# Performance work log

Hardware: AMD Instinct MI355X
Metric: run time of the kernel (lower is better)

The kernel has to match this reference:

```python
import jax, jax.numpy as jnp
import numpy as np

B, N, N_MELS = 8, 4096, 64
DIM, LAYERS, HEADS = 256, 4, 4
DIM_HEAD = DIM // HEADS      # 64
INNER = HEADS * DIM_HEAD     # 256
NB_FEAT = 256                # random features
FF_MULT = 4                  # performer_pytorch FeedForward default


def _ortho_projection(rows, cols, rng):
    # gaussian_orthogonal_random_matrix, scaling=0 (performer_pytorch default)
    blocks = []
    for _ in range((rows + cols - 1) // cols):
        q, _ = np.linalg.qr(rng.standard_normal((cols, cols)))
        blocks.append(q.T)
    mat = np.concatenate(blocks)[:rows]
    multiplier = np.linalg.norm(rng.standard_normal((rows, cols)), axis=1)
    return (mat * multiplier[:, None]).astype(np.float32)


def setup_inputs() -> dict:
    rng = np.random.default_rng(0)
    def w(*s, scale=0.02):
        return jnp.asarray(rng.standard_normal(s).astype(np.float32) * scale)
    G2 = 2 * DIM * FF_MULT  # GLU projection width = 2048
    return {
        "x": jnp.asarray(rng.standard_normal((B, N, N_MELS)).astype(np.float32)),
        "proj_w": w(N_MELS, DIM), "proj_b": jnp.zeros((DIM,), jnp.float32),
        "ln1_g": jnp.ones((LAYERS, DIM), jnp.float32), "ln1_b": jnp.zeros((LAYERS, DIM), jnp.float32),
        "wq": w(LAYERS, DIM, INNER), "bq": jnp.zeros((LAYERS, INNER), jnp.float32),
        "wk": w(LAYERS, DIM, INNER), "bk": jnp.zeros((LAYERS, INNER), jnp.float32),
        "wv": w(LAYERS, DIM, INNER), "bv": jnp.zeros((LAYERS, INNER), jnp.float32),
        "wo": w(LAYERS, INNER, DIM), "bo": jnp.zeros((LAYERS, DIM), jnp.float32),
        "ln2_g": jnp.ones((LAYERS, DIM), jnp.float32), "ln2_b": jnp.zeros((LAYERS, DIM), jnp.float32),
        "w1": w(LAYERS, DIM, G2), "b1": jnp.zeros((LAYERS, G2), jnp.float32),
        "w2": w(LAYERS, DIM * FF_MULT, DIM), "b2": jnp.zeros((LAYERS, DIM), jnp.float32),
        "clf_w": w(DIM, 1), "clf_b": jnp.zeros((1,), jnp.float32),
        "proj_mat": jnp.asarray(_ortho_projection(NB_FEAT, DIM_HEAD, rng)),
    }


def _layer_norm(x, g, b, eps=1e-5):
    mu = jnp.mean(x, -1, keepdims=True)
    var = jnp.mean((x - mu) ** 2, -1, keepdims=True)
    return (x - mu) * jax.lax.rsqrt(var + eps) * g + b


def _softmax_kernel(data, proj, is_query, eps=1e-4):
    # FAVOR+ positive random features for softmax (performer_pytorch.softmax_kernel)
    dn = data.shape[-1] ** -0.25          # data_normalizer
    ratio = proj.shape[0] ** -0.5
    dd = jnp.einsum('bhnd,md->bhnm', data * dn, proj)
    diag = jnp.sum(data ** 2, -1, keepdims=True) * 0.5 * (dn ** 2)
    if is_query:
        m = jax.lax.stop_gradient(jnp.max(dd, axis=-1, keepdims=True))
    else:
        m = jax.lax.stop_gradient(jnp.max(dd))
    return ratio * (jnp.exp(dd - diag - m) + eps)


def _split_heads(t):
    b, n, _ = t.shape
    return t.reshape(b, n, HEADS, DIM_HEAD).transpose(0, 2, 1, 3)  # b h n d


def _forward(x, proj_w, proj_b, ln1_g, ln1_b, wq, bq, wk, bk, wv, bv, wo, bo,
             ln2_g, ln2_b, w1, b1, w2, b2, clf_w, clf_b, proj_mat):
    h = x @ proj_w + proj_b                       # [B, N, DIM]
    b, n = h.shape[0], h.shape[1]
    for l in range(LAYERS):
        # --- pre-LN self-attention (FAVOR+, non-causal) ---
        y = _layer_norm(h, ln1_g[l], ln1_b[l])
        q = _split_heads(y @ wq[l] + bq[l])
        k = _split_heads(y @ wk[l] + bk[l])
        v = _split_heads(y @ wv[l] + bv[l])
        qp = _softmax_kernel(q, proj_mat, is_query=True)    # [b,h,n,m]
        kp = _softmax_kernel(k, proj_mat, is_query=False)   # [b,h,n,m]
        d_inv = 1.0 / jnp.einsum('bhnm,bhm->bhn', qp, kp.sum(axis=2))
        ctx = jnp.einsum('bhnm,bhnd->bhmd', kp, v)          # [b,h,m,d]
        o = jnp.einsum('bhmd,bhnm,bhn->bhnd', ctx, qp, d_inv)
        o = o.transpose(0, 2, 1, 3).reshape(b, n, INNER)
        h = h + (o @ wo[l] + bo[l])
        # --- pre-LN GLU feed-forward ---
        y = _layer_norm(h, ln2_g[l], ln2_b[l])
        u = y @ w1[l] + b1[l]
        a, g = jnp.split(u, 2, axis=-1)
        h = h + (jax.nn.gelu(a, approximate=False) * g) @ w2[l] + b2[l]
    # clf: transpose + AdaptiveAvgPool1d(1) == mean over time, then Linear(dim,1)
    pooled = h.mean(axis=1)                       # [B, DIM]
    return (pooled @ clf_w + clf_b)[:, 0]         # [B]


def reference(x, proj_w, proj_b, ln1_g, ln1_b, wq, bq, wk, bk, wv, bv, wo, bo,
              ln2_g, ln2_b, w1, b1, w2, b2, clf_w, clf_b, proj_mat):
    return _forward(x, proj_w, proj_b, ln1_g, ln1_b, wq, bq, wk, bk, wv, bv,
                    wo, bo, ln2_g, ln2_b, w1, b1, w2, b2, clf_w, clf_b, proj_mat)
```

## Files before the change

### kernel.cpp

```cpp
#include <hip/hip_runtime.h>
#include <cstdint>
#include <cstddef>

constexpr float DN = 0.35355339059327373f;
constexpr float RATIO = 0.0625f;
constexpr float EPSF = 1e-4f;

typedef __attribute__((ext_vector_type(8))) short short8;
typedef __attribute__((ext_vector_type(8))) _Float16 half8;
typedef __attribute__((ext_vector_type(4))) float f32x4;

constexpr size_t OFF_H     = 0;
constexpr size_t OFF_YS    = 33554432;
constexpr size_t OFF_WTS   = 50331648;
constexpr size_t OFF_QK    = 67108864;
constexpr size_t OFF_BIG   = 100663296;
constexpr size_t OFF_VT    = 167772160;
constexpr size_t OFF_CTXP  = 188743680;
constexpr size_t OFF_CTXTH = 199229440;
constexpr size_t OFF_DIAGQ = 201850880;
constexpr size_t OFF_DIAGK = 202375168;
constexpr size_t OFF_GMAX  = 203423744;
constexpr size_t OFF_POOL  = 203424000;
constexpr size_t OFF_PMTH  = 207749376;
constexpr size_t OFF_PWTH  = 207814912;
constexpr size_t OFF_PWTL  = 207847680;
constexpr size_t WS_BYTES  = 207880448;

constexpr size_t WQF = 0;
constexpr size_t WKF = 65536;
constexpr size_t WVF = 131072;
constexpr size_t WOF = 196608;
constexpr size_t W1F = 262144;
constexpr size_t W2F = 786432;

__device__ __forceinline__ unsigned fkey(float f) {
    unsigned u = __float_as_uint(f);
    return (u & 0x80000000u) ? ~u : (u | 0x80000000u);
}
__device__ __forceinline__ float funkey(unsigned k) {
    unsigned u = (k & 0x80000000u) ? (k ^ 0x80000000u) : ~k;
    return __uint_as_float(u);
}
__device__ __forceinline__ float gelu_exact(float x) {
    return 0.5f * x * (1.0f + erff(x * 0.70710678118654752f));
}
__device__ __forceinline__ void splitf(float x, unsigned short& h, unsigned short& l) {
    unsigned u = __float_as_uint(x);
    unsigned hv = (u + 0x7FFFu + ((u >> 16) & 1)) >> 16;
    h = (unsigned short)hv;
    float lo = x - __uint_as_float(hv << 16);
    unsigned u2 = __float_as_uint(lo);
    l = (unsigned short)((u2 + 0x7FFFu + ((u2 >> 16) & 1)) >> 16);
}
__device__ __forceinline__ unsigned short bf16rne(float x) {
    unsigned u = __float_as_uint(x);
    return (unsigned short)((u + 0x7FFFu + ((u >> 16) & 1)) >> 16);
}
__device__ __forceinline__ unsigned short fp16rne(float x) {
    return __builtin_bit_cast(unsigned short, (_Float16)x);
}
template<bool F16>
__device__ __forceinline__ f32x4 mfma16(short8 a, short8 b, f32x4 c) {
    if constexpr (F16)
        return __builtin_amdgcn_mfma_f32_16x16x32_f16(
            __builtin_bit_cast(half8, a), __builtin_bit_cast(half8, b), c, 0, 0, 0);
    else
        return __builtin_amdgcn_mfma_f32_16x16x32_bf16(a, b, c, 0, 0, 0);
}
__device__ __forceinline__ void xcd_swz(int& bx, int& by) {
    const int gx = gridDim.x;
    const int total = gx * gridDim.y;
    int flat = blockIdx.y * gx + blockIdx.x;
    flat = (flat & 7) * (total >> 3) + (flat >> 3);
    bx = flat % gx; by = flat / gx;
}

#if defined(__has_builtin)
#if __has_builtin(__builtin_amdgcn_global_load_lds)
#define HAVE_GLDS 1
#endif
#endif
__device__ __forceinline__ void glds16(const unsigned short* g, unsigned short* l) {
#ifdef HAVE_GLDS
    __builtin_amdgcn_global_load_lds(
        (const __attribute__((address_space(1))) unsigned int*)g,
        (__attribute__((address_space(3))) unsigned int*)l, 16, 0, 0);
#else
    *(uint4*)l = *(const uint4*)g;
#endif
}

__global__ void fill_sentinel(float* out, int n) {
    int i = threadIdx.x;
    if (i < n) out[i] = 12345.0f;
}
__global__ __launch_bounds__(256) void vt_init(unsigned short* __restrict__ vT, unsigned* __restrict__ gm) {
    int i = blockIdx.x * 256 + threadIdx.x;
    if (i < 4) gm[i] = 0u;
    const int bh = i >> 13;
    const int r = (i >> 9) & 15;
    const unsigned val = (r == 0) ? 0x3C003C00u : 0u;
    uint4 q; q.x = val; q.y = val; q.z = val; q.w = val;
    *(uint4*)(vT + ((size_t)bh * 80 + 64 + r) * 4096 + ((size_t)(i & 511) << 3)) = q;
}

__global__ __launch_bounds__(256) void split_scale(
    const float* __restrict__ src, unsigned short* __restrict__ hi,
    unsigned short* __restrict__ lo, int n, float scale)
{
    int i = blockIdx.x * 256 + threadIdx.x;
    if (i < n) {
        unsigned short h, l;
        splitf(src[i] * scale, h, l);
        hi[i] = h; lo[i] = l;
    }
}

__global__ __launch_bounds__(256) void tofp16_scale(
    const float* __restrict__ src, unsigned short* __restrict__ dst, int n, float scale)
{
    int i = blockIdx.x * 256 + threadIdx.x;
    if (i < n) dst[i] = fp16rne(src[i] * scale);
}

__global__ __launch_bounds__(256) void splitT(
    const float* __restrict__ W, unsigned short* __restrict__ hi,
    unsigned short* __restrict__ lo, int kshift, int N)
{
    int i = blockIdx.x * 256 + threadIdx.x;
    int K = 1 << kshift;
    int n = i >> kshift, k = i & (K - 1);
    unsigned short h, l;
    splitf(W[(size_t)k * N + n], h, l);
    hi[i] = h; lo[i] = l;
}

__global__ __launch_bounds__(256) void split_weights(
    const float* __restrict__ wq, const float* __restrict__ wk,
    const float* __restrict__ wv, const float* __restrict__ wo,
    const float* __restrict__ w1, const float* __restrict__ w2,
    unsigned short* __restrict__ dst)
{
    const int i = blockIdx.x * 256 + threadIdx.x;
    const int lay = i >> 20;
    const int r = i & 1048575;
    float val; size_t oh;
    if (r < 262144) {
        const int m = r >> 16, e = r & 65535;
        const int n = e >> 8, k = e & 255;
        const float* W = (m == 0 ? wq : m == 1 ? wk : m == 2 ? wv : wo);
        val = W[(size_t)lay * 65536 + k * 256 + n];
        oh = (size_t)lay * 1048576 + (size_t)m * 65536 + e;
    } else if (r < 786432) {
        const int e = r - 262144;
        const int n = e >> 8, k = e & 255;
        val = w1[(size_t)lay * 524288 + (size_t)k * 2048 + n];
        oh = (size_t)lay * 1048576 + W1F + e;
    } else {
        const int e = r - 786432;
        const int n = e >> 10, k = e & 1023;
        val = w2[(size_t)lay * 262144 + (size_t)k * 256 + n];
        oh = (size_t)lay * 1048576 + W2F + e;
    }
    dst[oh] = fp16rne(val);
}

__global__ __launch_bounds__(256) void ln_f16(
    const float* __restrict__ x, const float* __restrict__ g,
    const float* __restrict__ b, unsigned short* __restrict__ yhi)
{
    const int row = blockIdx.x * 4 + (threadIdx.x >> 6);
    const int lane = threadIdx.x & 63;
    float4 t = *(const float4*)&x[(size_t)row * 256 + lane * 4];
    float s = t.x + t.y + t.z + t.w;
#pragma unroll
    for (int sh = 1; sh < 64; sh <<= 1) s += __shfl_xor(s, sh);
    const float mu = s * (1.0f / 256.0f);
    const float dx = t.x - mu, dy = t.y - mu, dz = t.z - mu, dw = t.w - mu;
    float vv = dx * dx + dy * dy + dz * dz + dw * dw;
#pragma unroll
    for (int sh = 1; sh < 64; sh <<= 1) vv += __shfl_xor(vv, sh);
    const float rstd = rsqrtf(vv * (1.0f / 256.0f) + 1e-5f);
    float4 gv = *(const float4*)&g[lane * 4];
    float4 bv = *(const float4*)&b[lane * 4];
    unsigned short h0 = fp16rne(dx * rstd * gv.x + bv.x);
    unsigned short h1 = fp16rne(dy * rstd * gv.y + bv.y);
    unsigned short h2 = fp16rne(dz * rstd * gv.z + bv.z);
    unsigned short h3 = fp16rne(dw * rstd * gv.w + bv.w);
    uint2 ph;
    ph.x = (unsigned)h0 | ((unsigned)h1 << 16); ph.y = (unsigned)h2 | ((unsigned)h3 << 16);
    *(uint2*)&yhi[(size_t)row * 256 + lane * 4] = ph;
}

template<int EPI, bool ASPLIT, bool BSPLIT, bool F16>
__global__ __launch_bounds__(256) void gemm_mf(
    const unsigned short* __restrict__ Ahi, const unsigned short* __restrict__ Alo, int lda,
    const unsigned short* __restrict__ Bhi, const unsigned short* __restrict__ Blo, int ldb,
    int K,
    const float* __restrict__ bias, const float* __restrict__ res,
    float* __restrict__ C, int ldc,
    unsigned short* __restrict__ Obf,
    const float* __restrict__ diag, unsigned* __restrict__ keys)
{
    constexpr int NP = (ASPLIT ? 2 : 1) + (BSPLIT ? 2 : 1);
    constexpr int PB = ASPLIT ? 2 : 1;
    constexpr int NEED = (EPI == 6) ? 16384 : 0;
    constexpr int LDSN = (NP * 8192 > NEED) ? NP * 8192 : NEED;
    __shared__ unsigned short lds[LDSN];
    __shared__ float red[4];
#define LX(p, h, r, c) lds[(p) * 8192 + (h) * 4096 + (r) * 32 + (c)]
    int bx, by; xcd_swz(bx, by);
    const int tid = threadIdx.x;
    const int m0 = by * 128, n0 = bx * 128;
    const int sr = tid >> 2, sc = (tid & 3) * 8;
    const unsigned short* ga_h = Ahi + (size_t)(m0 + sr) * lda + sc;
    const unsigned short* ga_l = ASPLIT ? (Alo + (size_t)(m0 + sr) * lda + sc) : nullptr;
    const unsigned short* gb_h = Bhi + (size_t)(n0 + sr) * ldb + sc;
    const unsigned short* gb_l = BSPLIT ? (Blo + (size_t)(n0 + sr) * ldb + sc) : nullptr;
    unsigned short* lp = lds + tid * 8;
    const int l = tid & 63, w = tid >> 6;
    const int wr = (w >> 1) * 64, wc = (w & 1) * 64;
    const int fr = l & 15, fq = l >> 4;

    f32x4 acc[4][4];
#pragma unroll
    for (int i = 0; i < 4; ++i)
#pragma unroll
        for (int j = 0; j < 4; ++j) acc[i][j] = (f32x4){0.f, 0.f, 0.f, 0.f};

    for (int k0 = 0; k0 < K; k0 += 64) {
        glds16(ga_h + k0, lp);
        glds16(ga_h + (size_t)64 * lda + k0, lp + 2048);
        glds16(ga_h + k0 + 32, lp + 4096);
        glds16(ga_h + (size_t)64 * lda + k0 + 32, lp + 6144);
        if (ASPLIT) {
            glds16(ga_l + k0, lp + 8192);
            glds16(ga_l + (size_t)64 * lda + k0, lp + 10240);
            glds16(ga_l + k0 + 32, lp + 12288);
            glds16(ga_l + (size_t)64 * lda + k0 + 32, lp + 14336);
        }
        glds16(gb_h + k0, lp + PB * 8192);
        glds16(gb_h + (size_t)64 * ldb + k0, lp + PB * 8192 + 2048);
        glds16(gb_h + k0 + 32, lp + PB * 8192 + 4096);
        glds16(gb_h + (size_t)64 * ldb + k0 + 32, lp + PB * 8192 + 6144);
        if (BSPLIT) {
            glds16(gb_l + k0, lp + (PB + 1) * 8192);
            glds16(gb_l + (size_t)64 * ldb + k0, lp + (PB + 1) * 8192 + 2048);
            glds16(gb_l + k0 + 32, lp + (PB + 1) * 8192 + 4096);
            glds16(gb_l + (size_t)64 * ldb + k0 + 32, lp + (PB + 1) * 8192 + 6144);
        }
        __syncthreads();
#pragma unroll
        for (int h2 = 0; h2 < 2; ++h2) {
            short8 ah[4], al[4];
#pragma unroll
            for (int mf = 0; mf < 4; ++mf) {
                ah[mf] = *(const short8*)&LX(0, h2, wr + mf * 16 + fr, fq * 8);
                if (ASPLIT) al[mf] = *(const short8*)&LX(1, h2, wr + mf * 16 + fr, fq * 8);
            }
#pragma unroll
            for (int nf = 0; nf < 4; ++nf) {
                short8 bh = *(const short8*)&LX(PB, h2, wc + nf * 16 + fr, fq * 8);
#pragma unroll
                for (int mf = 0; mf < 4; ++mf) {
                    acc[mf][nf] = mfma16<F16>(ah[mf], bh, acc[mf][nf]);
                    if (ASPLIT) acc[mf][nf] = mfma16<F16>(al[mf], bh, acc[mf][nf]);
                }
                if (BSPLIT) {
                    short8 bl = *(const short8*)&LX(PB + 1, h2, wc + nf * 16 + fr, fq * 8);
#pragma unroll
                    for (int mf = 0; mf < 4; ++mf)
                        acc[mf][nf] = mfma16<F16>(ah[mf], bl, acc[mf][nf]);
                }
            }
        }
        __syncthreads();
    }

    if constexpr (EPI == 4) {
        float m = -3.4e38f;
#pragma unroll
        for (int mf = 0; mf < 4; ++mf)
#pragma unroll
            for (int nf = 0; nf < 4; ++nf)
#pragma unroll
                for (int v = 0; v < 4; ++v) m = fmaxf(m, acc[mf][nf][v]);
#pragma unroll
        for (int s = 1; s < 64; s <<= 1) m = fmaxf(m, __shfl_xor(m, s));
        if (l == 0) red[w] = m;
        __syncthreads();
        if (tid == 0)
            atomicMax(keys, fkey(fmaxf(fmaxf(red[0], red[1]), fmaxf(red[2], red[3]))));
    } else if constexpr (EPI == 6) {
        const float Mg = funkey(*keys);
        unsigned short* tb = lds;
#pragma unroll
        for (int mf = 0; mf < 4; ++mf)
#pragma unroll
            for (int v = 0; v < 4; ++v) {
                const int rl = wr + mf * 16 + fq * 4 + v;
                const float dg = diag[m0 + rl] + Mg;
#pragma unroll
                for (int nf = 0; nf < 4; ++nf) {
                    const int cl = wc + nf * 16 + fr;
                    tb[rl * 128 + cl] = fp16rne(RATIO * (__expf(acc[mf][nf][v] - dg) + EPSF));
                }
            }
        __syncthreads();
        const int tokbase = m0 >> 2;
        const int b = tokbase >> 12, nib = tokbase & 4095;
        const int ml = tid & 127, g2 = tid >> 7;
#pragma unroll
        for (int hh2 = 0; hh2 < 2; ++hh2) {
            const int hh = g2 * 2 + hh2;
            unsigned short* dst = Obf + ((size_t)((b * 4 + hh) * 256 + n0 + ml)) * 4096 + nib;
#pragma unroll
            for (int qq = 0; qq < 4; ++qq) {
                uint4 qv;
                unsigned wv[4];
#pragma unroll
                for (int j = 0; j < 4; ++j) {
                    unsigned s0 = tb[((qq * 8 + j * 2 + 0) * 4 + hh) * 128 + ml];
                    unsigned s1 = tb[((qq * 8 + j * 2 + 1) * 4 + hh) * 128 + ml];
                    wv[j] = s0 | (s1 << 16);
                }
                qv.x = wv[0]; qv.y = wv[1]; qv.z = wv[2]; qv.w = wv[3];
                *(uint4*)(dst + qq * 8) = qv;
            }
        }
    } else {
#pragma unroll
        for (int nf = 0; nf < 4; ++nf) {
            const int col = n0 + wc + nf * 16 + fr;
            float bb = 0.f;
            if (bias != nullptr) bb = bias[col];
#pragma unroll
            for (int mf = 0; mf < 4; ++mf) {
#pragma unroll
                for (int v = 0; v < 4; ++v) {
                    const int row = m0 + wr + mf * 16 + fq * 4 + v;
                    const size_t off = (size_t)row * ldc + col;
                    float val = acc[mf][nf][v] + bb;
                    if (EPI == 1) val += res[off];
                    C[off] = val;
                }
            }
        }
    }
#undef LX
}

__global__ __launch_bounds__(256) void gemm_qkv(
    const unsigned short* __restrict__ A, const unsigned short* __restrict__ wl,
    const float* __restrict__ bq, const float* __restrict__ bk, const float* __restrict__ bv,
    unsigned short* __restrict__ vT, unsigned short* __restrict__ khi,
    unsigned short* __restrict__ qhi, float* __restrict__ diagq, float* __restrict__ diagk)
{
    __shared__ unsigned short lds[16384];
    int bx, by; xcd_swz(bx, by);
    const int sel = by >> 8;
    const int m0 = (by & 255) * 128, n0 = bx * 128;
    const unsigned short* Bw = wl + (sel == 0 ? WVF : sel == 1 ? WKF : WQF);
    const float* bias = (sel == 0 ? bv : sel == 1 ? bk : bq);
    const int tid = threadIdx.x;
    const int sr = tid >> 2, sc = (tid & 3) * 8;
    const unsigned short* ga = A + (size_t)(m0 + sr) * 256 + sc;
    const unsigned short* gb = Bw + (size_t)(n0 + sr) * 256 + sc;
    unsigned short* lp = lds + tid * 8;
    const int l = tid & 63, w = tid >> 6;
    const int wr = (w >> 1) * 64, wc = (w & 1) * 64;
    const int fr = l & 15, fq = l >> 4;

    f32x4 acc[4][4];
#pragma unroll
    for (int i = 0; i < 4; ++i)
#pragma unroll
        for (int j = 0; j < 4; ++j) acc[i][j] = (f32x4){0.f, 0.f, 0.f, 0.f};

    for (int k0 = 0; k0 < 256; k0 += 64) {
        glds16(ga + k0, lp);
        glds16(ga + (size_t)64 * 256 + k0, lp + 2048);
        glds16(ga + k0 + 32, lp + 4096);
        glds16(ga + (size_t)64 * 256 + k0 + 32, lp + 6144);
        glds16(gb + k0, lp + 8192);
        glds16(gb + (size_t)64 * 256 + k0, lp + 10240);
        glds16(gb + k0 + 32, lp + 12288);
        glds16(gb + (size_t)64 * 256 + k0 + 32, lp + 14336);
        __syncthreads();
#pragma unroll
        for (int h2 = 0; h2 < 2; ++h2) {
            short8 ah[4];
#pragma unroll
            for (int mf = 0; mf < 4; ++mf)
                ah[mf] = *(const short8*)&lds[h2 * 4096 + (wr + mf * 16 + fr) * 32 + fq * 8];
#pragma unroll
            for (int nf = 0; nf < 4; ++nf) {
                short8 bh = *(const short8*)&lds[8192 + h2 * 4096 + (wc + nf * 16 + fr) * 32 + fq * 8];
#pragma unroll
                for (int mf = 0; mf < 4; ++mf)
                    acc[mf][nf] = mfma16<true>(ah[mf], bh, acc[mf][nf]);
            }
        }
        __syncthreads();
    }

    if (sel == 0) {
        unsigned short* tb = lds;
#pragma unroll
        for (int mf = 0; mf < 4; ++mf)
#pragma unroll
            for (int nf = 0; nf < 4; ++nf) {
                const int cl = wc + nf * 16 + fr;
                const float bb = bias[n0 + cl];
#pragma unroll
                for (int v = 0; v < 4; ++v) {
                    const int rl = wr + mf * 16 + fq * 4 + v;
                    tb[rl * 128 + cl] = fp16rne(acc[mf][nf][v] + bb);
                }
            }
        __syncthreads();
        const int b = m0 >> 12, nib = m0 & 4095;
        const int cl = tid & 127, half = tid >> 7;
        const int ch = n0 + cl, hh = ch >> 6, d = ch & 63;
        unsigned short* dst = vT + ((size_t)((b * 4 + hh) * 80 + d)) * 4096 + nib + half * 64;
#pragma unroll
        for (int qq = 0; qq < 8; ++qq) {
            uint4 qv;
            unsigned wv[4];
#pragma unroll
            for (int j = 0; j < 4; ++j) {
                unsigned s0 = tb[(half * 64 + qq * 8 + j * 2 + 0) * 128 + cl];
                unsigned s1 = tb[(half * 64 + qq * 8 + j * 2 + 1) * 128 + cl];
                wv[j] = s0 | (s1 << 16);
            }
            qv.x = wv[0]; qv.y = wv[1]; qv.z = wv[2]; qv.w = wv[3];
            *(uint4*)(dst + qq * 8) = qv;
        }
    } else {
        float* diag = (sel == 1 ? diagk : diagq);
        unsigned short* Obf = (sel == 1 ? khi : qhi);
        const int head = (n0 + wc) >> 6;
#pragma unroll
        for (int mf = 0; mf < 4; ++mf) {
            float sq[4] = {0.f, 0.f, 0.f, 0.f};
#pragma unroll
            for (int nf = 0; nf < 4; ++nf) {
                const int col = n0 + wc + nf * 16 + fr;
                const float bb = bias[col];
#pragma unroll
                for (int v = 0; v < 4; ++v) {
                    const int row = m0 + wr + mf * 16 + fq * 4 + v;
                    float val = acc[mf][nf][v] + bb;
                    Obf[(size_t)row * 256 + col] = fp16rne(val);
                    sq[v] += val * val;
                }
            }
#pragma unroll
            for (int v = 0; v < 4; ++v) {
                float s = sq[v];
                s += __shfl_xor(s, 1); s += __shfl_xor(s, 2);
                s += __shfl_xor(s, 4); s += __shfl_xor(s, 8);
                if (fr == 0)
                    diag[(size_t)(m0 + wr + mf * 16 + fq * 4 + v) * 4 + head] = s * 0.0625f;
            }
        }
    }
}

__global__ __launch_bounds__(256) void gemm_glu(
    const unsigned short* __restrict__ Ahi, const unsigned short* __restrict__ Wf,
    const float* __restrict__ b1, unsigned short* __restrict__ Obf)
{
    __shared__ unsigned short ldsA[8192];
    __shared__ unsigned short ldsB[8192];
    int bx, by; xcd_swz(bx, by);
    const int tid = threadIdx.x;
    const int m0 = by * 128, p0 = bx * 64;
    const int sr = tid >> 2, sc = (tid & 3) * 8;
    const unsigned short* ga  = Ahi + (size_t)(m0 + sr) * 256 + sc;
    const unsigned short* gba = Wf + (size_t)(p0 + sr) * 256 + sc;
    const unsigned short* gbg = Wf + (size_t)(1024 + p0 + sr) * 256 + sc;
    unsigned short* lpA = ldsA + tid * 8;
    unsigned short* lpB = ldsB + tid * 8;
    const int l = tid & 63, w = tid >> 6;
    const int wr = (w >> 1) * 64, wc = (w & 1) * 32;
    const int fr = l & 15, fq = l >> 4;

    f32x4 aa[4][2], ag[4][2];
#pragma unroll
    for (int i = 0; i < 4; ++i)
#pragma unroll
        for (int j = 0; j < 2; ++j) {
            aa[i][j] = (f32x4){0.f, 0.f, 0.f, 0.f};
            ag[i][j] = (f32x4){0.f, 0.f, 0.f, 0.f};
        }

    for (int k0 = 0; k0 < 256; k0 += 64) {
        glds16(ga + k0, lpA);
        glds16(ga + 64 * 256 + k0, lpA + 2048);
        glds16(ga + k0 + 32, lpA + 4096);
        glds16(ga + 64 * 256 + k0 + 32, lpA + 6144);
        glds16(gba + k0, lpB);
        glds16(gba + k0 + 32, lpB + 2048);
        glds16(gbg + k0, lpB + 4096);
        glds16(gbg + k0 + 32, lpB + 6144);
        __syncthreads();
#pragma unroll
        for (int h2 = 0; h2 < 2; ++h2) {
            short8 ah[4];
#pragma unroll
            for (int mf = 0; mf < 4; ++mf)
                ah[mf] = *(const short8*)&ldsA[h2 * 4096 + (wr + mf * 16 + fr) * 32 + fq * 8];
#pragma unroll
            for (int nf = 0; nf < 2; ++nf) {
                const int br_ = h2 * 2048 + (wc + nf * 16 + fr) * 32 + fq * 8;
                short8 bva = *(const short8*)&ldsB[br_];
                short8 bvg = *(const short8*)&ldsB[4096 + br_];
#pragma unroll
                for (int mf = 0; mf < 4; ++mf) {
                    aa[mf][nf] = mfma16<true>(ah[mf], bva, aa[mf][nf]);
                    ag[mf][nf] = mfma16<true>(ah[mf], bvg, ag[mf][nf]);
                }
            }
        }
        __syncthreads();
    }
#pragma unroll
    for (int nf = 0; nf < 2; ++nf) {
        const int ch = p0 + wc + nf * 16 + fr;
        const float ba = b1[ch], bg = b1[1024 + ch];
#pragma unroll
        for (int mf = 0; mf < 4; ++mf) {
#pragma unroll
            for (int v = 0; v < 4; ++v) {
                const int row = m0 + wr + mf * 16 + fq * 4 + v;
                float u = aa[mf][nf][v] + ba, g = ag[mf][nf][v] + bg;
                Obf[(size_t)row * 1024 + ch] = fp16rne(gelu_exact(u) * g);
            }
        }
    }
}

__global__ __launch_bounds__(256) void ctx_mfma(
    const unsigned short* __restrict__ kpT, const unsigned short* __restrict__ vT,
    float* __restrict__ ctxp)
{
    __shared__ unsigned short la[4096];
    __shared__ unsigned short lb[5120];
    int bx, by; xcd_swz(bx, by);
    const int bh = by, mt = bx & 3, kc = bx >> 2;
    const int tid = threadIdx.x;
    const int l = tid & 63, w = tid >> 6;
    const int wr = w * 16, fr = l & 15, fq = l >> 4;
    const int sr = tid >> 2, sc = (tid & 3) * 8;
    const unsigned short* ga  = kpT + ((size_t)bh * 256 + mt * 64 + sr) * 4096 + kc * 1024 + sc;
    const unsigned short* gb  = vT + ((size_t)bh * 80 + sr) * 4096 + kc * 1024 + sc;
    const unsigned short* gb2 = vT + ((size_t)bh * 80 + 64 + sr) * 4096 + kc * 1024 + sc;

    f32x4 acc[5];
#pragma unroll
    for (int j = 0; j < 5; ++j) acc[j] = (f32x4){0.f, 0.f, 0.f, 0.f};

    for (int k0 = 0; k0 < 1024; k0 += 64) {
        glds16(ga + k0, la + tid * 8);
        glds16(ga + k0 + 32, la + 2048 + tid * 8);
        glds16(gb + k0, lb + tid * 8);
        glds16(gb + k0 + 32, lb + 2560 + tid * 8);
        if (tid < 64) {
            glds16(gb2 + k0, lb + 2048 + tid * 8);
            glds16(gb2 + k0 + 32, lb + 2560 + 2048 + tid * 8);
        }
        __syncthreads();
#pragma unroll
        for (int h2 = 0; h2 < 2; ++h2) {
            short8 av = *(const short8*)&la[h2 * 2048 + (wr + fr) * 32 + fq * 8];
#pragma unroll
            for (int nf = 0; nf < 5; ++nf) {
                short8 bv = *(const short8*)&lb[h2 * 2560 + (nf * 16 + fr) * 32 + fq * 8];
                acc[nf] = mfma16<true>(av, bv, acc[nf]);
            }
        }
        __syncthreads();
    }
#pragma unroll
    for (int v = 0; v < 4; ++v) {
        const int row = mt * 64 + wr + fq * 4 + v;
#pragma unroll
        for (int nf = 0; nf < 5; ++nf)
            ctxp[((size_t)(kc * 32 + bh) * 256 + row) * 80 + nf * 16 + fr] = acc[nf][v];
    }
}

__global__ __launch_bounds__(256) void ctx_fix(
    const float* __restrict__ ctxp, unsigned short* __restrict__ cth)
{
    __shared__ float s[64][81];
    const int m0 = blockIdx.x * 64, bh = blockIdx.y;
    const int tid = threadIdx.x;
    for (int i = tid; i < 5120; i += 256) {
        const int ml = i / 80, dc = i % 80;
        float sum = 0.f;
#pragma unroll
        for (int kc = 0; kc < 4; ++kc)
            sum += ctxp[((size_t)(kc * 32 + bh) * 256 + m0 + ml) * 80 + dc];
        s[ml][dc] = sum;
    }
    __syncthreads();
    for (int i = tid; i < 5120; i += 256) {
        const int dc = i >> 6, ml = i & 63;
        cth[((size_t)bh * 80 + dc) * 256 + m0 + ml] = fp16rne(s[ml][dc]);
    }
}

__global__ __launch_bounds__(256) void qo_mfma(
    const unsigned short* __restrict__ qhi, const unsigned short* __restrict__ pmh,
    const unsigned short* __restrict__ cth, const float* __restrict__ diagq,
    unsigned short* __restrict__ osh)
{
    __shared__ unsigned short lds[16384 + 2560];
    __shared__ float rmax4[64][4];
    int bx, by; xcd_swz(bx, by);
    const int bh = by, b = bh >> 2, hh = bh & 3;
    const int t0 = bx * 64;
    const int tid = threadIdx.x;
    const int l = tid & 63, w = tid >> 6;
    const int fr = l & 15, fq = l >> 4;

    const int wc1 = w * 64;
    f32x4 a1[4][4];
#pragma unroll
    for (int i = 0; i < 4; ++i)
#pragma unroll
        for (int j = 0; j < 4; ++j) a1[i][j] = (f32x4){0.f, 0.f, 0.f, 0.f};

    const unsigned short* gq = qhi + (size_t)(b * 4096 + t0) * 256 + hh * 64;
#pragma unroll
    for (int ks = 0; ks < 2; ++ks) {
        const int k0 = ks * 32;
        glds16(gq + (size_t)(tid >> 2) * 256 + k0 + (tid & 3) * 8, lds + tid * 8);
#pragma unroll
        for (int i2 = 0; i2 < 4; ++i2) {
            const int c = tid + i2 * 256;
            glds16(pmh + (size_t)(c >> 2) * 64 + k0 + (c & 3) * 8, lds + 2048 + c * 8);
        }
        __syncthreads();
        short8 av[4];
#pragma unroll
        for (int mf = 0; mf < 4; ++mf)
            av[mf] = *(const short8*)&lds[(mf * 16 + fr) * 32 + fq * 8];
#pragma unroll
        for (int nf = 0; nf < 4; ++nf) {
            short8 bh_ = *(const short8*)&lds[2048 + (wc1 + nf * 16 + fr) * 32 + fq * 8];
#pragma unroll
            for (int mf = 0; mf < 4; ++mf)
                a1[mf][nf] = mfma16<true>(av[mf], bh_, a1[mf][nf]);
        }
        __syncthreads();
    }
#pragma unroll
    for (int mf = 0; mf < 4; ++mf)
#pragma unroll
        for (int v = 0; v < 4; ++v) {
            float rm = a1[mf][0][v];
#pragma unroll
            for (int nf = 1; nf < 4; ++nf) rm = fmaxf(rm, a1[mf][nf][v]);
            rm = fmaxf(rm, __shfl_xor(rm, 1));
            rm = fmaxf(rm, __shfl_xor(rm, 2));
            rm = fmaxf(rm, __shfl_xor(rm, 4));
            rm = fmaxf(rm, __shfl_xor(rm, 8));
            if (fr == 0) rmax4[mf * 16 + fq * 4 + v][w] = rm;
        }
    __syncthreads();
#pragma unroll
    for (int mf = 0; mf < 4; ++mf)
#pragma unroll
        for (int v = 0; v < 4; ++v) {
            const int tok = mf * 16 + fq * 4 + v;
            const float dg = diagq[(size_t)(b * 4096 + t0 + tok) * 4 + hh]
                           + fmaxf(fmaxf(rmax4[tok][0], rmax4[tok][1]),
                                   fmaxf(rmax4[tok][2], rmax4[tok][3]));
#pragma unroll
            for (int nf = 0; nf < 4; ++nf) {
                const int m = wc1 + nf * 16 + fr;
                lds[tok * 256 + (m ^ ((tok & 7) << 3))] =
                    fp16rne(RATIO * (__expf(a1[mf][nf][v] - dg) + EPSF));
            }
        }
    __syncthreads();

    unsigned short* lds2 = lds + 16384;
    f32x4 a2[5];
#pragma unroll
    for (int j = 0; j < 5; ++j) a2[j] = (f32x4){0.f, 0.f, 0.f, 0.f};
    const size_t bbase = (size_t)bh * 80 * 256;

    for (int k0 = 0; k0 < 256; k0 += 32) {
        glds16(cth + bbase + (size_t)(tid >> 2) * 256 + k0 + (tid & 3) * 8, lds2 + tid * 8);
        if (tid < 64) {
            const int c = 256 + tid;
            glds16(cth + bbase + (size_t)(c >> 2) * 256 + k0 + (c & 3) * 8, lds2 + c * 8);
        }
        __syncthreads();
        const int tok = w * 16 + fr;
        const int c = ((k0 >> 3) + fq) ^ (tok & 7);
        short8 av = *(const short8*)&lds[tok * 256 + c * 8];
#pragma unroll
        for (int nf = 0; nf < 5; ++nf) {
            short8 bvh = *(const short8*)&lds2[(nf * 16 + fr) * 32 + fq * 8];
            a2[nf] = mfma16<true>(av, bvh, a2[nf]);
        }
        __syncthreads();
    }
#pragma unroll
    for (int v = 0; v < 4; ++v) {
        const float den = __shfl(a2[4][v], (int)(l & 48));
        const float dinv = 1.0f / den;
        const int tok = w * 16 + fq * 4 + v;
        const size_t obase = (size_t)(b * 4096 + t0 + tok) * 256 + hh * 64;
#pragma unroll
        for (int nf = 0; nf < 4; ++nf)
            osh[obase + nf * 16 + fr] = fp16rne(a2[nf][v] * dinv);
    }
}

__global__ __launch_bounds__(256) void pool1_kernel(const float* __restrict__ h, float* __restrict__ part)
{
    const int b = blockIdx.x >> 4, ch = blockIdx.x & 15;
    const int tid = threadIdx.x;
    float acc = 0.f;
    for (int n = 0; n < 256; ++n)
        acc += h[((size_t)(b * 4096 + ch * 256 + n)) * 256 + tid];
    part[(size_t)blockIdx.x * 256 + tid] = acc;
}

__global__ __launch_bounds__(256) void pool2_kernel(
    const float* __restrict__ part, const float* __restrict__ cw,
    const float* __restrict__ cb, float* __restrict__ out)
{
    const int b = blockIdx.x, tid = threadIdx.x;
    float acc = 0.f;
#pragma unroll
    for (int c = 0; c < 16; ++c) acc += part[(size_t)(b * 16 + c) * 256 + tid];
    float val = acc * (1.0f / 4096.0f) * cw[tid];
#pragma unroll
    for (int s = 1; s < 64; s <<= 1) val += __shfl_xor(val, s);
    __shared__ float red[4];
    if ((tid & 63) == 0) red[tid >> 6] = val;
    __syncthreads();
    if (tid == 0) out[b] = red[0] + red[1] + red[2] + red[3] + cb[0];
}

extern "C" void kernel_launch(void* const* d_in, const int* in_sizes, int n_in,
                              void* d_out, int out_size, void* d_ws, size_t ws_size,
                              hipStream_t stream)
{
    (void)in_sizes; (void)n_in;
    if (ws_size < WS_BYTES) {
        fill_sentinel<<<1, 64, 0, stream>>>((float*)d_out, out_size);
        return;
    }

    const float* x     = (const float*)d_in[0];
    const float* projw = (const float*)d_in[1];
    const float* projb = (const float*)d_in[2];
    const float* ln1g  = (const float*)d_in[3];
    const float* ln1b  = (const float*)d_in[4];
    const float* wq    = (const float*)d_in[5];
    const float* bq    = (const float*)d_in[6];
    const float* wk    = (const float*)d_in[7];
    const float* bk    = (const float*)d_in[8];
    const float* wv    = (const float*)d_in[9];
    const float* bv    = (const float*)d_in[10];
    const float* wo    = (const float*)d_in[11];
    const float* bo    = (const float*)d_in[12];
    const float* ln2g  = (const float*)d_in[13];
    const float* ln2b  = (const float*)d_in[14];
    const float* w1    = (const float*)d_in[15];
    const float* b1    = (const float*)d_in[16];
    const float* w2    = (const float*)d_in[17];
    const float* b2    = (const float*)d_in[18];
    const float* clfw  = (const float*)d_in[19];
    const float* clfb  = (const float*)d_in[20];
    const float* projm = (const float*)d_in[21];

    char* WS = (char*)d_ws;
    float* h            = (float*)(WS + OFF_H);
    unsigned short* ysh = (unsigned short*)(WS + OFF_YS);
    unsigned short* wts = (unsigned short*)(WS + OFF_WTS);
    unsigned short* khi = (unsigned short*)(WS + OFF_QK);
    unsigned short* qhi = khi + 8388608;
    unsigned short* big = (unsigned short*)(WS + OFF_BIG);
    unsigned short* vT  = (unsigned short*)(WS + OFF_VT);
    float* ctxp         = (float*)(WS + OFF_CTXP);
    unsigned short* cth = (unsigned short*)(WS + OFF_CTXTH);
    float* diagq        = (float*)(WS + OFF_DIAGQ);
    float* diagk        = (float*)(WS + OFF_DIAGK);
    unsigned* gmax      = (unsigned*)(WS + OFF_GMAX);
    float* pool         = (float*)(WS + OFF_POOL);
    unsigned short* pmt_h = (unsigned short*)(WS + OFF_PMTH);
    unsigned short* pwt_h = (unsigned short*)(WS + OFF_PWTH);
    unsigned short* pwt_l = (unsigned short*)(WS + OFF_PWTL);
    unsigned short* xsh = big;
    unsigned short* xsl = big + 2097152;
    unsigned short* kpT = big;
    unsigned short* ffb = big;
    unsigned short* osh = ysh;

    split_scale<<<8192, 256, 0, stream>>>(x, xsh, xsl, 2097152, 1.0f);
    splitT<<<64, 256, 0, stream>>>(projw, pwt_h, pwt_l, 6, 256);
    tofp16_scale<<<64, 256, 0, stream>>>(projm, pmt_h, 16384, DN);
    vt_init<<<1024, 256, 0, stream>>>(vT, gmax);
    split_weights<<<16384, 256, 0, stream>>>(wq, wk, wv, wo, w1, w2, wts);
    gemm_mf<0, true, true, false><<<dim3(2, 256), 256, 0, stream>>>(xsh, xsl, 64,
        pwt_h, pwt_l, 64, 64, projb, nullptr, h, 256, nullptr, nullptr, nullptr);

    for (int l = 0; l < 4; ++l) {
        unsigned short* wl = wts + (size_t)l * 1048576;

        ln_f16<<<8192, 256, 0, stream>>>(h, ln1g + l * 256, ln1b + l * 256, ysh);
        gemm_qkv<<<dim3(2, 768), 256, 0, stream>>>(ysh, wl,
            bq + l * 256, bk + l * 256, bv + l * 256, vT, khi, qhi, diagq, diagk);
        gemm_mf<4, false, false, true><<<dim3(2, 1024), 256, 0, stream>>>(khi, nullptr, 64,
            pmt_h, nullptr, 64, 64, nullptr, nullptr, nullptr, 256, nullptr, nullptr, gmax + l);
        gemm_mf<6, false, false, true><<<dim3(2, 1024), 256, 0, stream>>>(khi, nullptr, 64,
            pmt_h, nullptr, 64, 64, nullptr, nullptr, nullptr, 256, kpT, diagk, gmax + l);
        ctx_mfma<<<dim3(16, 32), 256, 0, stream>>>(kpT, vT, ctxp);
        ctx_fix<<<dim3(4, 32), 256, 0, stream>>>(ctxp, cth);
        qo_mfma<<<dim3(64, 32), 256, 0, stream>>>(qhi, pmt_h, cth, diagq, osh);
        gemm_mf<1, false, false, true><<<dim3(2, 256), 256, 0, stream>>>(osh, nullptr, 256,
            wl + WOF, nullptr, 256, 256, bo + l * 256, h, h, 256, nullptr, nullptr, nullptr);

        ln_f16<<<8192, 256, 0, stream>>>(h, ln2g + l * 256, ln2b + l * 256, ysh);
        gemm_glu<<<dim3(16, 256), 256, 0, stream>>>(ysh, wl + W1F,
            b1 + (size_t)l * 2048, ffb);
        gemm_mf<1, false, false, true><<<dim3(2, 256), 256, 0, stream>>>(ffb, nullptr, 1024,
            wl + W2F, nullptr, 1024, 1024, b2 + l * 256, h, h, 256, nullptr, nullptr, nullptr);
    }

    pool1_kernel<<<128, 256, 0, stream>>>(h, pool);
    pool2_kernel<<<8, 256, 0, stream>>>(pool, clfw, clfb, (float*)d_out);
}
```

Before: 1.173 ms.

## Fuse residual GEMMs with following LayerNorm and use polynomial erf in GELU

Adds a 512-thread GEMM kernel that computes a full 128x256 row tile for the Wo and W2 projections, adds bias and residual, writes h, then reduces mean and variance across the tile in LDS and emits the next LayerNorm output as fp16. This removes the separate ln_f16 launches and their extra read of h inside the layer loop. GELU switches from erff to an Abramowitz-Stegun polynomial with __expf, which lowers the cost of the GLU epilogue but adds approximation error of roughly 1e-7. The residual path in the generic GEMM epilogue is dropped, and the last layer computes a LayerNorm that is never used.

```diff
diff --git a/kernel.cpp b/kernel.cpp
--- a/kernel.cpp
+++ b/kernel.cpp
@@ -42,8 +42,16 @@
     unsigned u = (k & 0x80000000u) ? (k ^ 0x80000000u) : ~k;
     return __uint_as_float(u);
 }
-__device__ __forceinline__ float gelu_exact(float x) {
-    return 0.5f * x * (1.0f + erff(x * 0.70710678118654752f));
+__device__ __forceinline__ float erf_fast(float x) {
+    float ax = fabsf(x);
+    float t = 1.0f / fmaf(0.3275911f, ax, 1.0f);
+    float p = t * fmaf(t, fmaf(t, fmaf(t, fmaf(t, 1.061405429f, -1.453152027f),
+                                      1.421413741f), -0.284496736f), 0.254829592f);
+    float r = 1.0f - p * __expf(-ax * ax);
+    return copysignf(r, x);
+}
+__device__ __forceinline__ float gelu_fast(float x) {
+    return 0.5f * x * (1.0f + erf_fast(x * 0.70710678118654752f));
 }
 __device__ __forceinline__ void splitf(float x, unsigned short& h, unsigned short& l) {
     unsigned u = __float_as_uint(x);
@@ -341,14 +349,127 @@
                 for (int v = 0; v < 4; ++v) {
                     const int row = m0 + wr + mf * 16 + fq * 4 + v;
                     const size_t off = (size_t)row * ldc + col;
-                    float val = acc[mf][nf][v] + bb;
-                    if (EPI == 1) val += res[off];
-                    C[off] = val;
+                    C[off] = acc[mf][nf][v] + bb;
                 }
             }
         }
     }
 #undef LX
+}
+
+__global__ __launch_bounds__(512) void gemm_w_ln(
+    const unsigned short* __restrict__ A, int lda, int K,
+    const unsigned short* __restrict__ W,
+    const float* __restrict__ bias, float* __restrict__ h,
+    const float* __restrict__ lng, const float* __restrict__ lnb,
+    unsigned short* __restrict__ ysh)
+{
+    __shared__ unsigned short ldsA[8192];
+    __shared__ unsigned short ldsB[16384];
+    int flat = blockIdx.x;
+    flat = (flat & 7) * ((int)gridDim.x >> 3) + (flat >> 3);
+    const int m0 = flat * 128;
+    const int tid = threadIdx.x;
+    const int sr = tid >> 2, sc = (tid & 3) * 8;
+    const unsigned short* ga = A + (size_t)(m0 + sr) * lda + sc;
+    const unsigned short* gb = W + (size_t)sr * K + sc;
+    unsigned short* lpA = ldsA + tid * 8;
+    const int l = tid & 63, w = tid >> 6;
+    const int wr = (w >> 2) * 64, wc = (w & 3) * 64;
+    const int fr = l & 15, fq = l >> 4;
+
+    f32x4 acc[4][4];
+#pragma unroll
+    for (int i = 0; i < 4; ++i)
+#pragma unroll
+        for (int j = 0; j < 4; ++j) acc[i][j] = (f32x4){0.f, 0.f, 0.f, 0.f};
+
+    for (int k0 = 0; k0 < K; k0 += 64) {
+        glds16(ga + k0, lpA);
+        glds16(ga + k0 + 32, lpA + 4096);
+        glds16(gb + k0, ldsB + tid * 8);
+        glds16(gb + (size_t)128 * K + k0, ldsB + 4096 + tid * 8);
+        glds16(gb + k0 + 32, ldsB + 8192 + tid * 8);
+        glds16(gb + (size_t)128 * K + k0 + 32, ldsB + 12288 + tid * 8);
+        __syncthreads();
+#pragma unroll
+        for (int h2 = 0; h2 < 2; ++h2) {
+            short8 ah[4];
+#pragma unroll
+            for (int mf = 0; mf < 4; ++mf)
+                ah[mf] = *(const short8*)&ldsA[h2 * 4096 + (wr + mf * 16 + fr) * 32 + fq * 8];
+#pragma unroll
+            for (int nf = 0; nf < 4; ++nf) {
+                short8 bv = *(const short8*)&ldsB[h2 * 8192 + (wc + nf * 16 + fr) * 32 + fq * 8];
+#pragma unroll
+                for (int mf = 0; mf < 4; ++mf)
+                    acc[mf][nf] = mfma16<true>(ah[mf], bv, acc[mf][nf]);
+            }
+        }
+        __syncthreads();
+    }
+
+    float* red = (float*)ldsA;
+#pragma unroll
+    for (int mf = 0; mf < 4; ++mf)
+#pragma unroll
+        for (int v = 0; v < 4; ++v) {
+            float s = 0.f;
+#pragma unroll
+            for (int nf = 0; nf < 4; ++nf) {
+                const int col = wc + nf * 16 + fr;
+                const int row = m0 + wr + mf * 16 + fq * 4 + v;
+                const size_t off = (size_t)row * 256 + col;
+                float val = acc[mf][nf][v] + bias[col] + h[off];
+                h[off] = val;
+                acc[mf][nf][v] = val;
+                s += val;
+            }
+            s += __shfl_xor(s, 1); s += __shfl_xor(s, 2);
+            s += __shfl_xor(s, 4); s += __shfl_xor(s, 8);
+            if (fr == 0) red[(wr + mf * 16 + fq * 4 + v) * 4 + (w & 3)] = s;
+        }
+    __syncthreads();
+    float mu[4][4];
+#pragma unroll
+    for (int mf = 0; mf < 4; ++mf)
+#pragma unroll
+        for (int v = 0; v < 4; ++v) {
+            const int rl = wr + mf * 16 + fq * 4 + v;
+            mu[mf][v] = (red[rl * 4] + red[rl * 4 + 1] + red[rl * 4 + 2] + red[rl * 4 + 3])
+                        * (1.0f / 256.0f);
+        }
+#pragma unroll
+    for (int mf = 0; mf < 4; ++mf)
+#pragma unroll
+        for (int v = 0; v < 4; ++v) {
+            float s = 0.f;
+#pragma unroll
+            for (int nf = 0; nf < 4; ++nf) {
+                const float d = acc[mf][nf][v] - mu[mf][v];
+                s += d * d;
+            }
+            s += __shfl_xor(s, 1); s += __shfl_xor(s, 2);
+            s += __shfl_xor(s, 4); s += __shfl_xor(s, 8);
+            if (fr == 0) red[512 + (wr + mf * 16 + fq * 4 + v) * 4 + (w & 3)] = s;
+        }
+    __syncthreads();
+#pragma unroll
+    for (int mf = 0; mf < 4; ++mf)
+#pragma unroll
+        for (int v = 0; v < 4; ++v) {
+            const int rl = wr + mf * 16 + fq * 4 + v;
+            const float var = (red[512 + rl * 4] + red[512 + rl * 4 + 1] +
+                               red[512 + rl * 4 + 2] + red[512 + rl * 4 + 3]) * (1.0f / 256.0f);
+            const float rstd = rsqrtf(var + 1e-5f);
+            const float m_ = mu[mf][v];
+#pragma unroll
+            for (int nf = 0; nf < 4; ++nf) {
+                const int col = wc + nf * 16 + fr;
+                ysh[(size_t)(m0 + rl) * 256 + col] =
+                    fp16rne((acc[mf][nf][v] - m_) * rstd * lng[col] + lnb[col]);
+            }
+        }
 }
 
 __global__ __launch_bounds__(256) void gemm_qkv(
@@ -536,7 +657,7 @@
             for (int v = 0; v < 4; ++v) {
                 const int row = m0 + wr + mf * 16 + fq * 4 + v;
                 float u = aa[mf][nf][v] + ba, g = ag[mf][nf][v] + bg;
-                Obf[(size_t)row * 1024 + ch] = fp16rne(gelu_exact(u) * g);
+                Obf[(size_t)row * 1024 + ch] = fp16rne(gelu_fast(u) * g);
             }
         }
     }
@@ -814,11 +935,11 @@
     split_weights<<<16384, 256, 0, stream>>>(wq, wk, wv, wo, w1, w2, wts);
     gemm_mf<0, true, true, false><<<dim3(2, 256), 256, 0, stream>>>(xsh, xsl, 64,
         pwt_h, pwt_l, 64, 64, projb, nullptr, h, 256, nullptr, nullptr, nullptr);
+    ln_f16<<<8192, 256, 0, stream>>>(h, ln1g, ln1b, ysh);
 
     for (int l = 0; l < 4; ++l) {
         unsigned short* wl = wts + (size_t)l * 1048576;
 
-        ln_f16<<<8192, 256, 0, stream>>>(h, ln1g + l * 256, ln1b + l * 256, ysh);
         gemm_qkv<<<dim3(2, 768), 256, 0, stream>>>(ysh, wl,
             bq + l * 256, bk + l * 256, bv + l * 256, vT, khi, qhi, diagq, diagk);
         gemm_mf<4, false, false, true><<<dim3(2, 1024), 256, 0, stream>>>(khi, nullptr, 64,
@@ -828,14 +949,15 @@
         ctx_mfma<<<dim3(16, 32), 256, 0, stream>>>(kpT, vT, ctxp);
         ctx_fix<<<dim3(4, 32), 256, 0, stream>>>(ctxp, cth);
         qo_mfma<<<dim3(64, 32), 256, 0, stream>>>(qhi, pmt_h, cth, diagq, osh);
-        gemm_mf<1, false, false, true><<<dim3(2, 256), 256, 0, stream>>>(osh, nullptr, 256,
-            wl + WOF, nullptr, 256, 256, bo + l * 256, h, h, 256, nullptr, nullptr, nullptr);
-
-        ln_f16<<<8192, 256, 0, stream>>>(h, ln2g + l * 256, ln2b + l * 256, ysh);
+        gemm_w_ln<<<256, 512, 0, stream>>>(osh, 256, 256, wl + WOF,
+            bo + l * 256, h, ln2g + l * 256, ln2b + l * 256, ysh);
+
         gemm_glu<<<dim3(16, 256), 256, 0, stream>>>(ysh, wl + W1F,
             b1 + (size_t)l * 2048, ffb);
-        gemm_mf<1, false, false, true><<<dim3(2, 256), 256, 0, stream>>>(ffb, nullptr, 1024,
-            wl + W2F, nullptr, 1024, 1024, b2 + l * 256, h, h, 256, nullptr, nullptr, nullptr);
+        const float* ng = (l < 3) ? (ln1g + (l + 1) * 256) : ln1g;
+        const float* nb = (l < 3) ? (ln1b + (l + 1) * 256) : ln1b;
+        gemm_w_ln<<<256, 512, 0, stream>>>(ffb, 1024, 1024, wl + W2F,
+            b2 + l * 256, h, ng, nb, ysh);
     }
 
     pool1_kernel<<<128, 256, 0, stream>>>(h, pool);
```

Result: slower. 1.201 ms (+2.4%).
